# Optimization experiments

Measured on AMD Instinct MI355X. Metric: run time of the kernel, lower is better.

## Reference

```python
import jax, jax.numpy as jnp
import numpy as np

HEADS = 8
DIM_HEAD = 64


def setup_inputs() -> dict:
    key = jax.random.key(0)
    ks = jax.random.split(key, 4)
    B, C, H, W = 1, 256, 64, 64
    inner = HEADS * DIM_HEAD  # 512
    x = jax.random.normal(ks[0], (B, C, H, W), dtype=jnp.float32)
    norm_w = jnp.ones((C,), dtype=jnp.float32)                      # RMSNorm weight (1,C,1,1) flattened
    w_qkv = jax.random.normal(ks[1], (3 * inner, C), dtype=jnp.float32) * 0.02  # 1x1 conv, no bias
    w_out = jax.random.normal(ks[2], (C, inner), dtype=jnp.float32) * 0.02      # 1x1 conv
    b_out = jax.random.normal(ks[3], (C,), dtype=jnp.float32) * 0.02
    return {"x": x, "norm_w": norm_w, "w_qkv": w_qkv, "w_out": w_out, "b_out": b_out}


def reference(x, norm_w, w_qkv, w_out, b_out):
    B, C, H, W = x.shape
    N = H * W
    # RMSNorm: F.normalize over channel dim (L2, eps clamp) * weight * sqrt(C)
    l2 = jnp.sqrt(jnp.sum(x * x, axis=1, keepdims=True))
    xn = x / jnp.maximum(l2, 1e-12) * norm_w[None, :, None, None] * (C ** 0.5)
    # 1x1 conv QKV = channel matmul
    qkv = jnp.einsum('oc,bchw->bohw', w_qkv, xn)  # [B, 3*inner, H, W]
    q, k, v = jnp.split(qkv, 3, axis=1)

    def split_heads(t):
        # 'b (h d) x y -> b h (x y) d'
        return t.reshape(B, HEADS, DIM_HEAD, N).transpose(0, 1, 3, 2)

    q, k, v = map(split_heads, (q, k, v))
    scale = DIM_HEAD ** -0.5
    scores = jnp.einsum('bhnd,bhmd->bhnm', q, k) * scale  # [B,H,N,N]
    attn = jax.nn.softmax(scores, axis=-1)
    out = jnp.einsum('bhnm,bhmd->bhnd', attn, v)
    # 'b h (x y) d -> b (h d) x y'
    out = out.transpose(0, 1, 3, 2).reshape(B, HEADS * DIM_HEAD, H, W)
    # output 1x1 conv + residual (note: residual is the NORMALIZED x, per source)
    return jnp.einsum('ci,bihw->bchw', w_out, out) + b_out[None, :, None, None] + xn
```

## Files before the change

kernel.cpp:

```cpp
#include <hip/hip_runtime.h>


#define NPIX 4096
#define CIN 256
#define INNER 512
#define NHEAD 8
#define DH 64

typedef _Float16 f16;
typedef __attribute__((ext_vector_type(8))) _Float16 f16x8;
typedef __attribute__((ext_vector_type(4))) float f32x4;

static __device__ __forceinline__ f32x4 mfma_f16(f16x8 a, f16x8 b, f32x4 c) {
  return __builtin_amdgcn_mfma_f32_16x16x32_f16(a, b, c, 0, 0, 0);
}

static __device__ __forceinline__ unsigned pk2(float lo, float hi) {
  return __builtin_bit_cast(unsigned, __builtin_amdgcn_cvt_pkrtz(lo, hi));
}

static __device__ __forceinline__ void gload_lds16(const void* g, void* l) {
  __builtin_amdgcn_global_load_lds(
      (const __attribute__((address_space(1))) unsigned*)g,
      (__attribute__((address_space(3))) unsigned*)l, 16, 0, 0);
}

__global__ __launch_bounds__(256) void k_cvt2(const float* __restrict__ a1, int n1,
                                              const float* __restrict__ a2, int n2,
                                              f16* __restrict__ b) {
  int i = blockIdx.x * 256 + threadIdx.x;
  if (i < n1) b[i] = (f16)a1[i];
  else if (i < n1 + n2) b[i] = (f16)a2[i - n1];
}

__global__ __launch_bounds__(256) void k_rmsnorm(const float* __restrict__ x,
                                                 const float* __restrict__ w,
                                                 float* __restrict__ xn,
                                                 f16* __restrict__ xnT) {
  const int pi = threadIdx.x & 15, cs = threadIdx.x >> 4;
  const int p = blockIdx.x * 16 + pi;
  __shared__ float red[16][16];
  float xv[16];
  float ss = 0.f;
#pragma unroll
  for (int i = 0; i < 16; ++i) {
    xv[i] = x[(cs * 16 + i) * NPIX + p];
    ss += xv[i] * xv[i];
  }
  red[cs][pi] = ss;
  __syncthreads();
  float tot = 0.f;
#pragma unroll
  for (int s = 0; s < 16; ++s) tot += red[s][pi];
  float inv = 16.0f / fmaxf(sqrtf(tot), 1e-12f);
  union { f16x8 v[2]; f16 h[16]; } hv;
#pragma unroll
  for (int i = 0; i < 16; ++i) {
    int c = cs * 16 + i;
    float v = xv[i] * inv * w[c];
    xn[c * NPIX + p] = v;
    hv.h[i] = (f16)v;
  }
  *(f16x8*)(xnT + (size_t)p * CIN + cs * 16) = hv.v[0];
  *(f16x8*)(xnT + (size_t)p * CIN + cs * 16 + 8) = hv.v[1];
}

__global__ __launch_bounds__(256) void k_qkv(const f16* __restrict__ wqkv,
                                             const f16* __restrict__ xnT,
                                             f16* __restrict__ qT,
                                             f16* __restrict__ kT,
                                             f16* __restrict__ vv) {
  const int lane = threadIdx.x & 63, wave = threadIdx.x >> 6;
  const int l15 = lane & 15, quad = lane >> 4;
  const int obase = blockIdx.y * 64 + (wave >> 1) * 32;
  const int pbase = blockIdx.x * 128 + (wave & 1) * 64;
  const int sect = blockIdx.y >> 3;
  f32x4 acc[8];
#pragma unroll
  for (int i = 0; i < 8; ++i) acc[i] = (f32x4){0.f, 0.f, 0.f, 0.f};
#pragma unroll
  for (int kc = 0; kc < CIN / 32; ++kc) {
    f16x8 af[2], bfr[4];
#pragma unroll
    for (int oc = 0; oc < 2; ++oc)
      af[oc] = *(const f16x8*)(wqkv + (size_t)(obase + oc * 16 + l15) * CIN + kc * 32 + quad * 8);
#pragma unroll
    for (int pc = 0; pc < 4; ++pc)
      bfr[pc] = *(const f16x8*)(xnT + (size_t)(pbase + pc * 16 + l15) * CIN + kc * 32 + quad * 8);
    if (sect < 2) {
#pragma unroll
      for (int pc = 0; pc < 4; ++pc)
#pragma unroll
        for (int oc = 0; oc < 2; ++oc)
          acc[pc * 2 + oc] = mfma_f16(bfr[pc], af[oc], acc[pc * 2 + oc]);
    } else {
#pragma unroll
      for (int oc = 0; oc < 2; ++oc)
#pragma unroll
        for (int pc = 0; pc < 4; ++pc)
          acc[oc * 4 + pc] = mfma_f16(af[oc], bfr[pc], acc[oc * 4 + pc]);
    }
  }
  if (sect < 2) {
    f16* dst = (sect == 0) ? qT : kT;
    const float sc = (sect == 0) ? 0.18033688f : 1.0f;
    const int head = blockIdx.y & 7;
    const int dd = (wave >> 1) * 32;
#pragma unroll
    for (int pc = 0; pc < 4; ++pc)
#pragma unroll
      for (int oc = 0; oc < 2; ++oc)
#pragma unroll
        for (int r = 0; r < 4; ++r) {
          int p = pbase + pc * 16 + quad * 4 + r;
          dst[((size_t)(head << 12) + p) * DH + dd + oc * 16 + l15] =
              (f16)(acc[pc * 2 + oc][r] * sc);
        }
  } else {
#pragma unroll
    for (int oc = 0; oc < 2; ++oc)
#pragma unroll
      for (int r = 0; r < 4; ++r) {
        int o = obase + oc * 16 + quad * 4 + r - 2 * INNER;
#pragma unroll
        for (int pc = 0; pc < 4; ++pc)
          vv[(size_t)o * NPIX + pbase + pc * 16 + l15] = (f16)acc[oc * 4 + pc][r];
      }
  }
}

template <typename PT>
__global__ __launch_bounds__(256, 4) void k_attn(const f16* __restrict__ qT,
                                                 const f16* __restrict__ kT,
                                                 const f16* __restrict__ vv,
                                                 PT* __restrict__ Opart,
                                                 float* __restrict__ Lpart) {
  const int bid = blockIdx.x;
  const int head = bid & 7, split = (bid >> 3) & 3, qb = bid >> 5;
  const int tid = threadIdx.x;
  const int wave = tid >> 6, lane = tid & 63;
  const int l15 = lane & 15, quad = lane >> 4;
  const int keybase = split * 1024;

  __shared__ f16 KV[2][8192];

  const int qrow = (head << 12) + qb * 128 + wave * 32;
  f16x8 qf[2][2];
#pragma unroll
  for (int qt = 0; qt < 2; ++qt)
#pragma unroll
    for (int kc = 0; kc < 2; ++kc)
      qf[qt][kc] = *(const f16x8*)(qT + (size_t)(qrow + qt * 16 + l15) * DH + kc * 32 + quad * 8);

  f32x4 o[2][4];
  float ol[2] = {0.f, 0.f};
#pragma unroll
  for (int qt = 0; qt < 2; ++qt)
#pragma unroll
    for (int c = 0; c < 4; ++c) o[qt][c] = (f32x4){0.f, 0.f, 0.f, 0.f};

  const int sKey8 = lane >> 3;
  const int sCol = lane & 7;
  const int rx = l15 & 7;
  const int srcA4 = (((quad & 1) << 5) + l15) * 4;
  const int srcB4 = srcA4 + 64;
  const bool hiQuad = quad >= 2;

  auto stage = [&](int ch, int b) {
    const int R0 = wave * 4096;
#pragma unroll
    for (int j = 0; j < 4; ++j) {
      const int Rb = R0 + j * 1024;
      char* ldst = (char*)(&KV[b][0]) + Rb;
      if (Rb < 8192) {
        const int key = (Rb >> 7) + sKey8;
        const f16* src = kT + ((size_t)(head << 12) + keybase + ch * 64 + key) * DH +
                         ((sCol ^ (key & 7)) << 3);
        gload_lds16(src, ldst);
      } else {
        const int dd = ((Rb - 8192) >> 7) + sKey8;
        const f16* src = vv + ((size_t)(head * DH) + dd) * NPIX + keybase + ch * 64 +
                         ((sCol ^ (dd & 7)) << 3);
        gload_lds16(src, ldst);
      }
    }
  };

  stage(0, 0);
  __syncthreads();

  for (int ch = 0; ch < 16; ++ch) {
    const int b = ch & 1;
    if (ch < 15) stage(ch + 1, b ^ 1);
    const f16* Kb = &KV[b][0];
    const f16* Vb = &KV[b][4096];
#pragma unroll
    for (int h = 0; h < 2; ++h) {
      f16x8 kf[2][2], vf[4];
#pragma unroll
      for (int nc = 0; nc < 2; ++nc) {
        const int key = h * 32 + nc * 16 + l15;
#pragma unroll
        for (int kc = 0; kc < 2; ++kc)
          kf[nc][kc] = *(const f16x8*)(Kb + key * 64 + (((kc * 4 + quad) ^ rx) << 3));
      }
#pragma unroll
      for (int c = 0; c < 4; ++c) {
        const int dd = c * 16 + l15;
        vf[c] = *(const f16x8*)(Vb + dd * 64 + (((h * 4 + quad) ^ rx) << 3));
      }
#pragma unroll
      for (int qt = 0; qt < 2; ++qt) {
        f32x4 s0 = mfma_f16(kf[0][0], qf[qt][0], (f32x4){0.f, 0.f, 0.f, 0.f});
        s0 = mfma_f16(kf[0][1], qf[qt][1], s0);
        f32x4 s1 = mfma_f16(kf[1][0], qf[qt][0], (f32x4){0.f, 0.f, 0.f, 0.f});
        s1 = mfma_f16(kf[1][1], qf[qt][1], s1);
        float p0[4], p1[4];
#pragma unroll
        for (int r = 0; r < 4; ++r) {
          p0[r] = __builtin_amdgcn_exp2f(s0[r]);
          p1[r] = __builtin_amdgcn_exp2f(s1[r]);
        }
        ol[qt] += ((p0[0] + p0[1]) + (p0[2] + p0[3])) +
                  ((p1[0] + p1[1]) + (p1[2] + p1[3]));
        unsigned A0 = pk2(p0[0], p0[1]), B0 = pk2(p0[2], p0[3]);
        unsigned A1 = pk2(p1[0], p1[1]), B1 = pk2(p1[2], p1[3]);
        unsigned As = hiQuad ? A1 : A0;
        unsigned Bs = hiQuad ? B1 : B0;
        union { f16x8 v; unsigned u[4]; } pf;
        pf.u[0] = (unsigned)__builtin_amdgcn_ds_bpermute(srcA4, (int)As);
        pf.u[1] = (unsigned)__builtin_amdgcn_ds_bpermute(srcA4, (int)Bs);
        pf.u[2] = (unsigned)__builtin_amdgcn_ds_bpermute(srcB4, (int)As);
        pf.u[3] = (unsigned)__builtin_amdgcn_ds_bpermute(srcB4, (int)Bs);
#pragma unroll
        for (int c = 0; c < 4; ++c) o[qt][c] = mfma_f16(vf[c], pf.v, o[qt][c]);
      }
    }
    __syncthreads();
  }

#pragma unroll
  for (int qt = 0; qt < 2; ++qt) {
    ol[qt] += __shfl_xor(ol[qt], 16);
    ol[qt] += __shfl_xor(ol[qt], 32);
  }

#pragma unroll
  for (int qt = 0; qt < 2; ++qt) {
#pragma unroll
    for (int c = 0; c < 4; ++c)
#pragma unroll
      for (int r = 0; r < 4; ++r)
        Opart[((size_t)split * 32768 + qrow + qt * 16 + l15) * 64 + c * 16 + quad * 4 + r] =
            (PT)o[qt][c][r];
    if (quad == 0) Lpart[split * 32768 + qrow + qt * 16 + l15] = ol[qt];
  }
}

template <typename PT>
__global__ __launch_bounds__(256) void k_merge(const PT* __restrict__ Opart,
                                               const float* __restrict__ Lpart,
                                               f16* __restrict__ Ows) {
  const int tg = blockIdx.x * 256 + threadIdx.x;
  const int qi = tg >> 2;
  const size_t base = (size_t)tg * 16;
  float acc[16];
#pragma unroll
  for (int i = 0; i < 16; ++i) acc[i] = 0.f;
  float L = 0.f;
#pragma unroll
  for (int s = 0; s < 4; ++s) {
    const PT* p = Opart + (size_t)s * (32768 * 64) + base;
    if constexpr (sizeof(PT) == 4) {
      const float4* p4 = (const float4*)p;
      float4 v0 = p4[0], v1 = p4[1], v2 = p4[2], v3 = p4[3];
      acc[0] += v0.x; acc[1] += v0.y; acc[2] += v0.z; acc[3] += v0.w;
      acc[4] += v1.x; acc[5] += v1.y; acc[6] += v1.z; acc[7] += v1.w;
      acc[8] += v2.x; acc[9] += v2.y; acc[10] += v2.z; acc[11] += v2.w;
      acc[12] += v3.x; acc[13] += v3.y; acc[14] += v3.z; acc[15] += v3.w;
    } else {
      const f16x8* ph = (const f16x8*)p;
      f16x8 v0 = ph[0], v1 = ph[1];
#pragma unroll
      for (int i = 0; i < 8; ++i) {
        acc[i] += (float)v0[i];
        acc[8 + i] += (float)v1[i];
      }
    }
    L += Lpart[s * 32768 + qi];
  }
  union { f16x8 v[2]; f16 h[16]; } hv;
#pragma unroll
  for (int i = 0; i < 16; ++i) hv.h[i] = (f16)(acc[i] / L);
  *(f16x8*)(Ows + base) = hv.v[0];
  *(f16x8*)(Ows + base + 8) = hv.v[1];
}

__global__ __launch_bounds__(256) void k_oproj(const f16* __restrict__ wout,
                                               const f16* __restrict__ Ows,
                                               const float* __restrict__ bout,
                                               const float* __restrict__ xn,
                                               float* __restrict__ out) {
  const int lane = threadIdx.x & 63, wave = threadIdx.x >> 6;
  const int l15 = lane & 15, quad = lane >> 4;
  const int mbase = blockIdx.y * 32 + (wave >> 1) * 16;
  const int pbase = blockIdx.x * 64 + (wave & 1) * 32;
  f32x4 acc[2];
  acc[0] = (f32x4){0.f, 0.f, 0.f, 0.f};
  acc[1] = (f32x4){0.f, 0.f, 0.f, 0.f};
#pragma unroll
  for (int kc = 0; kc < INNER / 32; ++kc) {
    f16x8 af = *(const f16x8*)(wout + (size_t)(mbase + l15) * INNER + kc * 32 + quad * 8);
    int i0 = kc * 32 + quad * 8;
    int head = i0 >> 6, d0 = i0 & 63;
#pragma unroll
    for (int pc = 0; pc < 2; ++pc) {
      f16x8 bfr = *(const f16x8*)(Ows + ((size_t)(head << 12) + pbase + pc * 16 + l15) * DH + d0);
      acc[pc] = mfma_f16(af, bfr, acc[pc]);
    }
  }
#pragma unroll
  for (int pc = 0; pc < 2; ++pc)
#pragma unroll
    for (int r = 0; r < 4; ++r) {
      int c = mbase + quad * 4 + r, p = pbase + pc * 16 + l15;
      out[c * NPIX + p] = acc[pc][r] + bout[c] + xn[c * NPIX + p];
    }
}

extern "C" void kernel_launch(void* const* d_in, const int* in_sizes, int n_in,
                              void* d_out, int out_size, void* d_ws, size_t ws_size,
                              hipStream_t stream) {
  (void)in_sizes; (void)n_in; (void)out_size;
  const float* x      = (const float*)d_in[0];
  const float* norm_w = (const float*)d_in[1];
  const float* w_qkv  = (const float*)d_in[2];
  const float* w_out  = (const float*)d_in[3];
  const float* b_out  = (const float*)d_in[4];
  float* out = (float*)d_out;

  char* ws = (char*)d_ws;
  float* xn    = (float*)(ws);
  f16* xnT     = (f16*)(ws + (4u << 20));
  f16* qT      = (f16*)(ws + (6u << 20));
  f16* kT      = (f16*)(ws + (10u << 20));
  f16* vv      = (f16*)(ws + (14u << 20));
  f16* Ows     = (f16*)(ws + (18u << 20));
  f16* wqkv_h  = (f16*)(ws + (22u << 20));
  f16* wout_h  = (f16*)(ws + (22u << 20) + 786432);

  const int n1 = 3 * INNER * CIN, n2 = CIN * INNER;
  hipLaunchKernelGGL(k_cvt2, dim3((n1 + n2 + 255) / 256), dim3(256), 0, stream,
                     w_qkv, n1, w_out, n2, wqkv_h);
  hipLaunchKernelGGL(k_rmsnorm, dim3(NPIX / 16), dim3(256), 0, stream, x, norm_w, xn, xnT);
  hipLaunchKernelGGL(k_qkv, dim3(NPIX / 128, 1536 / 64), dim3(256), 0, stream,
                     wqkv_h, xnT, qT, kT, vv);

  const size_t OPLANE = (size_t)32768 * 64;
  char* pbase = ws + (24u << 20);
  if (ws_size >= (24u << 20) + OPLANE * 4 * sizeof(float) + 4 * 32768 * sizeof(float)) {
    float* Op = (float*)pbase;
    float* Lp = (float*)(pbase + OPLANE * 4 * sizeof(float));
    hipLaunchKernelGGL((k_attn<float>), dim3(1024), dim3(256), 0, stream,
                       qT, kT, vv, Op, Lp);
    hipLaunchKernelGGL((k_merge<float>), dim3(512), dim3(256), 0, stream,
                       Op, Lp, Ows);
  } else {
    f16* Op = (f16*)pbase;
    float* Lp = (float*)(pbase + OPLANE * 4 * sizeof(f16));
    hipLaunchKernelGGL((k_attn<f16>), dim3(1024), dim3(256), 0, stream,
                       qT, kT, vv, Op, Lp);
    hipLaunchKernelGGL((k_merge<f16>), dim3(512), dim3(256), 0, stream,
                       Op, Lp, Ows);
  }

  hipLaunchKernelGGL(k_oproj, dim3(NPIX / 64, CIN / 32), dim3(256), 0, stream,
                     wout_h, Ows, b_out, xn, out);
}
```

Baseline: 154.8 us.

## Double per-wave query tile and swap bpermute for permlane swaps in attention

Each wave now handles 64 query rows instead of 32, which halves the block count to 512 and lets each K/V chunk staged in LDS be reused across twice as many queries. The ds_bpermute shuffle that turned P into an MFMA operand is replaced with v_permlane16/32_swap register instructions, avoiding LDS-path latency. Staging pointers are precomputed and advanced by a fixed step, and fp32 partial outputs are written as float4 stores. In exchange the kernel uses more registers (occupancy hint lowered to 2) and exposes less block-level parallelism.

New measurement: 153.4 us. No clear change (-0.9%).

```diff
diff --git a/kernel.cpp b/kernel.cpp
--- a/kernel.cpp
+++ b/kernel.cpp
@@ -130,7 +130,7 @@
 }
 
 template <typename PT>
-__global__ __launch_bounds__(256, 4) void k_attn(const f16* __restrict__ qT,
+__global__ __launch_bounds__(256, 2) void k_attn(const f16* __restrict__ qT,
                                                  const f16* __restrict__ kT,
                                                  const f16* __restrict__ vv,
                                                  PT* __restrict__ Opart,
@@ -144,54 +144,53 @@
 
   __shared__ f16 KV[2][8192];
 
-  const int qrow = (head << 12) + qb * 128 + wave * 32;
-  f16x8 qf[2][2];
-#pragma unroll
-  for (int qt = 0; qt < 2; ++qt)
+  const int qrow = (head << 12) + qb * 256 + wave * 64;
+  f16x8 qf[4][2];
+#pragma unroll
+  for (int qt = 0; qt < 4; ++qt)
 #pragma unroll
     for (int kc = 0; kc < 2; ++kc)
       qf[qt][kc] = *(const f16x8*)(qT + (size_t)(qrow + qt * 16 + l15) * DH + kc * 32 + quad * 8);
 
-  f32x4 o[2][4];
-  float ol[2] = {0.f, 0.f};
-#pragma unroll
-  for (int qt = 0; qt < 2; ++qt)
+  f32x4 o[4][4];
+  float ol[4] = {0.f, 0.f, 0.f, 0.f};
+#pragma unroll
+  for (int qt = 0; qt < 4; ++qt)
 #pragma unroll
     for (int c = 0; c < 4; ++c) o[qt][c] = (f32x4){0.f, 0.f, 0.f, 0.f};
 
-  const int sKey8 = lane >> 3;
-  const int sCol = lane & 7;
   const int rx = l15 & 7;
-  const int srcA4 = (((quad & 1) << 5) + l15) * 4;
-  const int srcB4 = srcA4 + 64;
-  const bool hiQuad = quad >= 2;
-
-  auto stage = [&](int ch, int b) {
-    const int R0 = wave * 4096;
+  const bool qodd = (quad & 1) != 0;
+
+  const int sRow8 = lane >> 3, sCol = lane & 7;
+  const f16* sp[4];
+  const int step = (wave < 2) ? 64 * DH : 64;
+#pragma unroll
+  for (int j = 0; j < 4; ++j) {
+    const int Rb = wave * 4096 + j * 1024;
+    if (wave < 2) {
+      const int key = (Rb >> 7) + sRow8;
+      sp[j] = kT + ((size_t)(head << 12) + keybase + key) * DH + ((sCol ^ (key & 7)) << 3);
+    } else {
+      const int dd = ((Rb - 8192) >> 7) + sRow8;
+      sp[j] = vv + ((size_t)(head * DH) + dd) * NPIX + keybase + ((sCol ^ (dd & 7)) << 3);
+    }
+  }
+  auto stage = [&](int b) {
+    char* base = (char*)(&KV[b][0]) + wave * 4096;
 #pragma unroll
     for (int j = 0; j < 4; ++j) {
-      const int Rb = R0 + j * 1024;
-      char* ldst = (char*)(&KV[b][0]) + Rb;
-      if (Rb < 8192) {
-        const int key = (Rb >> 7) + sKey8;
-        const f16* src = kT + ((size_t)(head << 12) + keybase + ch * 64 + key) * DH +
-                         ((sCol ^ (key & 7)) << 3);
-        gload_lds16(src, ldst);
-      } else {
-        const int dd = ((Rb - 8192) >> 7) + sKey8;
-        const f16* src = vv + ((size_t)(head * DH) + dd) * NPIX + keybase + ch * 64 +
-                         ((sCol ^ (dd & 7)) << 3);
-        gload_lds16(src, ldst);
-      }
+      gload_lds16(sp[j], base + j * 1024);
+      sp[j] += step;
     }
   };
 
-  stage(0, 0);
+  stage(0);
   __syncthreads();
 
   for (int ch = 0; ch < 16; ++ch) {
     const int b = ch & 1;
-    if (ch < 15) stage(ch + 1, b ^ 1);
+    if (ch < 15) stage(b ^ 1);
     const f16* Kb = &KV[b][0];
     const f16* Vb = &KV[b][4096];
 #pragma unroll
@@ -210,7 +209,7 @@
         vf[c] = *(const f16x8*)(Vb + dd * 64 + (((h * 4 + quad) ^ rx) << 3));
       }
 #pragma unroll
-      for (int qt = 0; qt < 2; ++qt) {
+      for (int qt = 0; qt < 4; ++qt) {
         f32x4 s0 = mfma_f16(kf[0][0], qf[qt][0], (f32x4){0.f, 0.f, 0.f, 0.f});
         s0 = mfma_f16(kf[0][1], qf[qt][1], s0);
         f32x4 s1 = mfma_f16(kf[1][0], qf[qt][0], (f32x4){0.f, 0.f, 0.f, 0.f});
@@ -225,13 +224,21 @@
                   ((p1[0] + p1[1]) + (p1[2] + p1[3]));
         unsigned A0 = pk2(p0[0], p0[1]), B0 = pk2(p0[2], p0[3]);
         unsigned A1 = pk2(p1[0], p1[1]), B1 = pk2(p1[2], p1[3]);
-        unsigned As = hiQuad ? A1 : A0;
-        unsigned Bs = hiQuad ? B1 : B0;
+        asm("v_permlane16_swap_b32 %0, %1" : "+v"(A0), "+v"(A1));
+        asm("v_permlane16_swap_b32 %0, %1" : "+v"(B0), "+v"(B1));
+        unsigned xa = A0, ya = A0;
+        asm("v_permlane32_swap_b32 %0, %1" : "+v"(xa), "+v"(ya));
+        unsigned xa2 = A1, ya2 = A1;
+        asm("v_permlane32_swap_b32 %0, %1" : "+v"(xa2), "+v"(ya2));
+        unsigned xb = B0, yb = B0;
+        asm("v_permlane32_swap_b32 %0, %1" : "+v"(xb), "+v"(yb));
+        unsigned xb2 = B1, yb2 = B1;
+        asm("v_permlane32_swap_b32 %0, %1" : "+v"(xb2), "+v"(yb2));
         union { f16x8 v; unsigned u[4]; } pf;
-        pf.u[0] = (unsigned)__builtin_amdgcn_ds_bpermute(srcA4, (int)As);
-        pf.u[1] = (unsigned)__builtin_amdgcn_ds_bpermute(srcA4, (int)Bs);
-        pf.u[2] = (unsigned)__builtin_amdgcn_ds_bpermute(srcB4, (int)As);
-        pf.u[3] = (unsigned)__builtin_amdgcn_ds_bpermute(srcB4, (int)Bs);
+        pf.u[0] = qodd ? ya : xa;
+        pf.u[1] = qodd ? yb : xb;
+        pf.u[2] = qodd ? ya2 : xa2;
+        pf.u[3] = qodd ? yb2 : xb2;
 #pragma unroll
         for (int c = 0; c < 4; ++c) o[qt][c] = mfma_f16(vf[c], pf.v, o[qt][c]);
       }
@@ -240,19 +247,25 @@
   }
 
 #pragma unroll
-  for (int qt = 0; qt < 2; ++qt) {
+  for (int qt = 0; qt < 4; ++qt) {
     ol[qt] += __shfl_xor(ol[qt], 16);
     ol[qt] += __shfl_xor(ol[qt], 32);
   }
 
 #pragma unroll
-  for (int qt = 0; qt < 2; ++qt) {
-#pragma unroll
-    for (int c = 0; c < 4; ++c)
-#pragma unroll
-      for (int r = 0; r < 4; ++r)
-        Opart[((size_t)split * 32768 + qrow + qt * 16 + l15) * 64 + c * 16 + quad * 4 + r] =
-            (PT)o[qt][c][r];
+  for (int qt = 0; qt < 4; ++qt) {
+#pragma unroll
+    for (int c = 0; c < 4; ++c) {
+      const size_t off =
+          ((size_t)split * 32768 + qrow + qt * 16 + l15) * 64 + c * 16 + quad * 4;
+      if constexpr (sizeof(PT) == 4) {
+        *(float4*)(Opart + off) =
+            make_float4(o[qt][c][0], o[qt][c][1], o[qt][c][2], o[qt][c][3]);
+      } else {
+#pragma unroll
+        for (int r = 0; r < 4; ++r) Opart[off + r] = (PT)o[qt][c][r];
+      }
+    }
     if (quad == 0) Lpart[split * 32768 + qrow + qt * 16 + l15] = ol[qt];
   }
 }
@@ -361,14 +374,14 @@
   if (ws_size >= (24u << 20) + OPLANE * 4 * sizeof(float) + 4 * 32768 * sizeof(float)) {
     float* Op = (float*)pbase;
     float* Lp = (float*)(pbase + OPLANE * 4 * sizeof(float));
-    hipLaunchKernelGGL((k_attn<float>), dim3(1024), dim3(256), 0, stream,
+    hipLaunchKernelGGL((k_attn<float>), dim3(512), dim3(256), 0, stream,
                        qT, kT, vv, Op, Lp);
     hipLaunchKernelGGL((k_merge<float>), dim3(512), dim3(256), 0, stream,
                        Op, Lp, Ows);
   } else {
     f16* Op = (f16*)pbase;
     float* Lp = (float*)(pbase + OPLANE * 4 * sizeof(f16));
-    hipLaunchKernelGGL((k_attn<f16>), dim3(1024), dim3(256), 0, stream,
+    hipLaunchKernelGGL((k_attn<f16>), dim3(512), dim3(256), 0, stream,
                        qT, kT, vv, Op, Lp);
     hipLaunchKernelGGL((k_merge<f16>), dim3(512), dim3(256), 0, stream,
                        Op, Lp, Ows);
```
